# Kernel tuning notes

Hardware: AMD Instinct MI355X
Metric: run time of the kernel (lower is better)

## Reference

```python
import jax, jax.numpy as jnp
import numpy as np

H = 16  # num heads

def setup_inputs() -> dict:
    key = jax.random.key(0)
    k1, k2, k3 = jax.random.split(key, 3)
    B, L, D = 2, 2048, 1024
    x = jax.random.normal(k1, (B, L, D), dtype=jnp.float32)
    # torch Linear weight is [out,in]; we store transposed [in,out] so y = x @ W
    w_qkv = jax.random.normal(k2, (D, 3 * D), dtype=jnp.float32) * (D ** -0.5)
    w_proj = jax.random.normal(k3, (D, D), dtype=jnp.float32) * (D ** -0.5)
    return {"x": x, "w_qkv": w_qkv, "w_proj": w_proj, "num_prefix_tokens": 256}

def _prefix_causal_mask(L: int, M: int):
    # True = masked. Strict upper triangle (causal), then text rows (M:) may
    # see ALL prefix columns (:M).
    mask = jnp.triu(jnp.ones((L, L), dtype=bool), k=1)
    mask = mask.at[M:, :M].set(False)
    return mask

def reference(x, w_qkv, w_proj, num_prefix_tokens):
    B, L, D = x.shape
    d = D // H
    scale = d ** -0.5
    qkv = (x @ w_qkv).reshape(B, L, 3, H, d)
    q = jnp.transpose(qkv[:, :, 0], (0, 2, 1, 3))  # [B,H,L,d]
    k = jnp.transpose(qkv[:, :, 1], (0, 2, 1, 3))
    v = jnp.transpose(qkv[:, :, 2], (0, 2, 1, 3))
    logits = jnp.einsum("bhqd,bhkd->bhqk", q, k) * scale  # [B,H,L,L]
    mask = _prefix_causal_mask(L, num_prefix_tokens)
    logits = jnp.where(mask[None, None], -jnp.inf, logits)
    attn = jax.nn.softmax(logits, axis=-1)
    out = jnp.einsum("bhqk,bhkd->bhqd", attn, v)  # [B,H,L,d]
    out = jnp.transpose(out, (0, 2, 1, 3)).reshape(B, L, D)
    return out @ w_proj
```

## Files before the change

kernel.cpp:

```cpp
#include <hip/hip_runtime.h>
#include <hip/hip_bf16.h>

#define BATCH   2
#define L_SEQ   2048
#define DMODEL  1024
#define NHEADS  16
#define DHEAD   64
#define SEG     (BATCH*NHEADS*L_SEQ*DHEAD)

typedef __attribute__((ext_vector_type(8)))  short bf16x8;
typedef __attribute__((ext_vector_type(4)))  float f32x4;
typedef __attribute__((ext_vector_type(16))) float f32x16;

__device__ __forceinline__ unsigned short f2b(float f) {
    unsigned int u = __float_as_uint(f);
    return (unsigned short)((u + 0x7FFFu + ((u >> 16) & 1u)) >> 16);
}
__device__ __forceinline__ unsigned int pk2(float a, float b) {
    __hip_bfloat162 h = __float22bfloat162_rn(make_float2(a, b));
    return *(unsigned int*)&h;
}
__device__ __forceinline__ void glds16(const unsigned short* g, unsigned short* l) {
    __builtin_amdgcn_global_load_lds(
        (const __attribute__((address_space(1))) unsigned int*)g,
        (__attribute__((address_space(3))) unsigned int*)l, 16, 0, 0);
}

__device__ __forceinline__ void tcast64(const float* __restrict__ in,
                                        unsigned short* __restrict__ out,
                                        int K, int N, int bx, int by, int t) {
    __shared__ unsigned short T[64][65];
    const int k0 = by * 64, n0 = bx * 64;
    const int r = t >> 4, c4 = (t & 15) * 4;
#pragma unroll
    for (int rep = 0; rep < 4; ++rep) {
        int kk = rep * 16 + r;
        float4 f = *(const float4*)&in[(size_t)(k0 + kk) * N + n0 + c4];
        T[kk][c4 + 0] = f2b(f.x);
        T[kk][c4 + 1] = f2b(f.y);
        T[kk][c4 + 2] = f2b(f.z);
        T[kk][c4 + 3] = f2b(f.w);
    }
    __syncthreads();
#pragma unroll
    for (int rep = 0; rep < 4; ++rep) {
        int nn = rep * 16 + r;
        ushort4 o;
        o.x = T[c4 + 0][nn];
        o.y = T[c4 + 1][nn];
        o.z = T[c4 + 2][nn];
        o.w = T[c4 + 3][nn];
        *(ushort4*)&out[(size_t)(n0 + nn) * K + k0 + c4] = o;
    }
}

__global__ __launch_bounds__(256)
void prep(const float* __restrict__ x, const float* __restrict__ wqkv,
          const float* __restrict__ wproj, unsigned short* __restrict__ xb,
          unsigned short* __restrict__ wqkvT, unsigned short* __restrict__ wprojT) {
    const int id = blockIdx.x, t = threadIdx.x;
    if (id < 4096) {
        int i = id * 1024 + t * 4;
        float4 f = *(const float4*)&x[i];
        ushort4 o;
        o.x = f2b(f.x); o.y = f2b(f.y); o.z = f2b(f.z); o.w = f2b(f.w);
        *(ushort4*)&xb[i] = o;
    } else if (id < 4864) {
        int lid = id - 4096;
        tcast64(wqkv, wqkvT, DMODEL, 3 * DMODEL, lid % 48, lid / 48, t);
    } else {
        int lid = id - 4864;
        tcast64(wproj, wprojT, DMODEL, DMODEL, lid & 15, lid >> 4, t);
    }
}

__global__ __launch_bounds__(256)
void gemm_qkv(const unsigned short* __restrict__ A, const unsigned short* __restrict__ Bt,
              unsigned short* __restrict__ Cb) {
    __shared__ unsigned short SLDS[2 * 128 * 128];

    const int t = threadIdx.x;
    const int lane = t & 63, wave = t >> 6;
    const int quad = lane >> 4, l16 = lane & 15;
    const int wm = (wave >> 1) * 64, wn = (wave & 1) * 64;
    const int id = blockIdx.y * gridDim.x + blockIdx.x;
    const int xcd = id & 7, sq = id >> 3;
    const int m0 = (xcd * 4 + sq / 24) * 128;
    const int n0 = (sq % 24) * 128;
    const bool vrole = (n0 >= 2048);

    const int gsw = (lane & 7) ^ (lane >> 3);
    const unsigned short* ga[4];
    const unsigned short* gb[4];
    int ldA[4], ldB[4];
#pragma unroll
    for (int i = 0; i < 4; ++i) {
        int row = wave * 32 + i * 8 + (lane >> 3);
        ga[i] = &A[(size_t)(m0 + row) * DMODEL + gsw * 8];
        gb[i] = &Bt[(size_t)(n0 + row) * DMODEL + gsw * 8];
        ldA[i] = (wave * 32 + i * 8) * 64;
        ldB[i] = 8192 + (wave * 32 + i * 8) * 64;
    }
    const int sx = l16 & 7;

    f32x4 acc[4][4];
#pragma unroll
    for (int i = 0; i < 4; ++i)
#pragma unroll
        for (int j = 0; j < 4; ++j)
#pragma unroll
            for (int r = 0; r < 4; ++r) acc[i][j][r] = 0.0f;

#pragma unroll
    for (int i = 0; i < 4; ++i) {
        glds16(ga[i], &SLDS[ldA[i]]);
        glds16(gb[i], &SLDS[ldB[i]]);
    }
    __syncthreads();

    int cur = 0;
    for (int kt = 0; kt < 16; ++kt) {
        if (kt < 15) {
            const int ko = (kt + 1) * 64;
            unsigned short* dst = &SLDS[(cur ^ 1) * 16384];
#pragma unroll
            for (int i = 0; i < 4; ++i) {
                glds16(ga[i] + ko, dst + ldA[i]);
                glds16(gb[i] + ko, dst + ldB[i]);
            }
        }
        const unsigned short* Asm = &SLDS[cur * 16384];
        const unsigned short* Bsm = Asm + 8192;
#pragma unroll
        for (int s = 0; s < 2; ++s) {
            bf16x8 af[4], bfr[4];
#pragma unroll
            for (int i = 0; i < 4; ++i)
                af[i] = *(const bf16x8*)&Asm[(wm + i * 16 + l16) * 64 + ((4 * s + quad) ^ sx) * 8];
#pragma unroll
            for (int j = 0; j < 4; ++j)
                bfr[j] = *(const bf16x8*)&Bsm[(wn + j * 16 + l16) * 64 + ((4 * s + quad) ^ sx) * 8];
            __builtin_amdgcn_s_setprio(1);
            if (!vrole) {
#pragma unroll
                for (int i = 0; i < 4; ++i)
#pragma unroll
                    for (int j = 0; j < 4; ++j)
                        acc[i][j] = __builtin_amdgcn_mfma_f32_16x16x32_bf16(af[i], bfr[j], acc[i][j], 0, 0, 0);
            } else {
#pragma unroll
                for (int i = 0; i < 4; ++i)
#pragma unroll
                    for (int j = 0; j < 4; ++j)
                        acc[i][j] = __builtin_amdgcn_mfma_f32_16x16x32_bf16(bfr[j], af[i], acc[i][j], 0, 0, 0);
            }
            __builtin_amdgcn_s_setprio(0);
        }
        __syncthreads();
        cur ^= 1;
    }

    const float qscale = 0.1803368801111244f;
    const float scl = (!vrole && n0 < 1024) ? qscale : 1.0f;
#pragma unroll
    for (int i = 0; i < 4; ++i)
#pragma unroll
        for (int r = 0; r < 4; ++r) {
#pragma unroll
            for (int j = 0; j < 4; ++j) {
                int row_l, col_l;
                if (!vrole) {
                    row_l = wm + i * 16 + quad * 4 + r;
                    col_l = wn + j * 16 + l16;
                } else {
                    row_l = wn + j * 16 + quad * 4 + r;
                    col_l = wm + i * 16 + l16;
                }
                int key = row_l & 7;
                SLDS[row_l * 128 + (((col_l >> 3) ^ key) * 8) + (col_l & 7)] =
                    f2b(acc[i][j][r] * scl);
            }
        }
    __syncthreads();

    const int s0 = n0 >> 10;
    const int bb = m0 >> 11;
#pragma unroll
    for (int it = 0; it < 4; ++it) {
        int row = it * 32 + (t >> 3);
        int c = t & 7;
        int key = row & 7;
        bf16x8 v0 = *(const bf16x8*)&SLDS[row * 128 + ((c ^ key) * 8)];
        bf16x8 v1 = *(const bf16x8*)&SLDS[row * 128 + (((c + 8) ^ key) * 8)];
        if (!vrole) {
            int token = m0 + row, lp = token & (L_SEQ - 1);
            int n_a = n0 + c * 8,        h_a = (n_a >> 6) & 15, d_a = n_a & 63;
            int n_b = n0 + (c + 8) * 8,  h_b = (n_b >> 6) & 15, d_b = n_b & 63;
            size_t base = (size_t)s0 * SEG;
            *(bf16x8*)&Cb[base + (((size_t)(bb * NHEADS + h_a) * L_SEQ + lp) * DHEAD) + d_a] = v0;
            *(bf16x8*)&Cb[base + (((size_t)(bb * NHEADS + h_b) * L_SEQ + lp) * DHEAD) + d_b] = v1;
        } else {
            int fr = (n0 - 2048) + row;
            int h = fr >> 6, dd = fr & 63;
            int lp0 = (m0 & (L_SEQ - 1));
            size_t base = 2 * (size_t)SEG +
                          (((size_t)(bb * NHEADS + h) * DHEAD + dd) * L_SEQ) + lp0;
            *(bf16x8*)&Cb[base + c * 8]       = v0;
            *(bf16x8*)&Cb[base + (c + 8) * 8] = v1;
        }
    }
}

__global__ __launch_bounds__(256)
void gemm_proj(const unsigned short* __restrict__ A, const unsigned short* __restrict__ Bt,
               float* __restrict__ Cf) {
    __shared__ unsigned short SLDS[2 * 128 * 128];

    const int t = threadIdx.x;
    const int lane = t & 63, wave = t >> 6;
    const int quad = lane >> 4, l16 = lane & 15;
    const int wm = (wave >> 1) * 64, wn = (wave & 1) * 64;
    const int id = blockIdx.y * gridDim.x + blockIdx.x;
    const int xcd = id & 7, sq = id >> 3;
    const int m0 = (xcd * 4 + (sq >> 3)) * 128;
    const int n0 = (sq & 7) * 128;

    const int gsw = (lane & 7) ^ (lane >> 3);
    const unsigned short* ga[4];
    const unsigned short* gb[4];
    int ldA[4], ldB[4];
#pragma unroll
    for (int i = 0; i < 4; ++i) {
        int row = wave * 32 + i * 8 + (lane >> 3);
        ga[i] = &A[(size_t)(m0 + row) * DMODEL + gsw * 8];
        gb[i] = &Bt[(size_t)(n0 + row) * DMODEL + gsw * 8];
        ldA[i] = (wave * 32 + i * 8) * 64;
        ldB[i] = 8192 + (wave * 32 + i * 8) * 64;
    }
    const int sx = l16 & 7;

    f32x4 acc[4][4];
#pragma unroll
    for (int i = 0; i < 4; ++i)
#pragma unroll
        for (int j = 0; j < 4; ++j)
#pragma unroll
            for (int r = 0; r < 4; ++r) acc[i][j][r] = 0.0f;

#pragma unroll
    for (int i = 0; i < 4; ++i) {
        glds16(ga[i], &SLDS[ldA[i]]);
        glds16(gb[i], &SLDS[ldB[i]]);
    }
    __syncthreads();

    int cur = 0;
    for (int kt = 0; kt < 16; ++kt) {
        if (kt < 15) {
            const int ko = (kt + 1) * 64;
            unsigned short* dst = &SLDS[(cur ^ 1) * 16384];
#pragma unroll
            for (int i = 0; i < 4; ++i) {
                glds16(ga[i] + ko, dst + ldA[i]);
                glds16(gb[i] + ko, dst + ldB[i]);
            }
        }
        const unsigned short* Asm = &SLDS[cur * 16384];
        const unsigned short* Bsm = Asm + 8192;
#pragma unroll
        for (int s = 0; s < 2; ++s) {
            bf16x8 af[4], bfr[4];
#pragma unroll
            for (int i = 0; i < 4; ++i)
                af[i] = *(const bf16x8*)&Asm[(wm + i * 16 + l16) * 64 + ((4 * s + quad) ^ sx) * 8];
#pragma unroll
            for (int j = 0; j < 4; ++j)
                bfr[j] = *(const bf16x8*)&Bsm[(wn + j * 16 + l16) * 64 + ((4 * s + quad) ^ sx) * 8];
            __builtin_amdgcn_s_setprio(1);
#pragma unroll
            for (int i = 0; i < 4; ++i)
#pragma unroll
                for (int j = 0; j < 4; ++j)
                    acc[i][j] = __builtin_amdgcn_mfma_f32_16x16x32_bf16(af[i], bfr[j], acc[i][j], 0, 0, 0);
            __builtin_amdgcn_s_setprio(0);
        }
        __syncthreads();
        cur ^= 1;
    }

#pragma unroll
    for (int i = 0; i < 4; ++i)
#pragma unroll
        for (int r = 0; r < 4; ++r) {
            int row = m0 + wm + i * 16 + quad * 4 + r;
#pragma unroll
            for (int j = 0; j < 4; ++j)
                Cf[(size_t)row * DMODEL + n0 + wn + j * 16 + l16] = acc[i][j][r];
        }
}

__global__ __launch_bounds__(512)
void attn_mfma(const unsigned short* __restrict__ Qg, const unsigned short* __restrict__ Kg,
               const unsigned short* __restrict__ Vg, unsigned short* __restrict__ Ao) {
    __shared__ unsigned short SLDS[32768];
    __shared__ float Rex[128];
    unsigned short* Ksm = SLDS;
    unsigned short* Vsm = SLDS + 8192;
    unsigned short* Psm = SLDS + 16384;

    const int t = threadIdx.x;
    const int lane = t & 63, wave = t >> 6;
    const int l31 = lane & 31, hi = lane >> 5;
    const int bh = blockIdx.x & 31;
    const int Qt = 15 - (blockIdx.x >> 5);
    const int q0 = Qt * 128;
    const int qh = wave & 3, kp = wave >> 2;
    const int wq0 = q0 + qh * 32;
    const int nstrip = Qt + 1;
    const int b = bh >> 4, h = bh & 15;
    const size_t qkbase = (size_t)bh * L_SEQ * DHEAD;
    const size_t vbase  = (size_t)bh * DHEAD * L_SEQ;

    bf16x8 bq[4];
#pragma unroll
    for (int ks = 0; ks < 4; ++ks)
        bq[ks] = *(const bf16x8*)&Qg[qkbase + (size_t)(wq0 + l31) * DHEAD + ks * 16 + hi * 8];

    const int kc0 = t & 7,  kr0 = (t >> 3) * 2;
    const int vc0 = t & 15, vd0 = (t >> 4) * 2;

    unsigned short* Pw = Psm + wave * 2048;

    f32x16 O0, O1;
#pragma unroll
    for (int r = 0; r < 16; ++r) { O0[r] = 0.0f; O1[r] = 0.0f; }
    float rs = 0.0f;

    bf16x8 gk[2], gv[2];
#pragma unroll
    for (int i = 0; i < 2; ++i) {
        gk[i] = *(const bf16x8*)&Kg[qkbase + (size_t)(kr0 + i) * DHEAD + kc0 * 8];
        gv[i] = *(const bf16x8*)&Vg[vbase + (size_t)(vd0 + i) * L_SEQ + vc0 * 8];
    }

    for (int s = 0; s < nstrip; ++s) {
        __syncthreads();
#pragma unroll
        for (int i = 0; i < 2; ++i) {
            *(bf16x8*)&Ksm[(kc0 * 128 + ((kr0 + i) ^ kc0)) * 8] = gk[i];
            *(bf16x8*)&Vsm[(vc0 * 64 + ((vd0 + i) ^ vc0)) * 8] = gv[i];
        }
        if (s + 1 < nstrip) {
            const int kn = (s + 1) * 128;
#pragma unroll
            for (int i = 0; i < 2; ++i) {
                gk[i] = *(const bf16x8*)&Kg[qkbase + (size_t)(kn + kr0 + i) * DHEAD + kc0 * 8];
                gv[i] = *(const bf16x8*)&Vg[vbase + (size_t)(vd0 + i) * L_SEQ + kn + vc0 * 8];
            }
        }
        __syncthreads();

        const int keybase = s * 128 + kp * 64;
        if (keybase <= wq0 + 31) {
            f32x16 ST[2];
            __builtin_amdgcn_s_setprio(1);
#pragma unroll
            for (int kh = 0; kh < 2; ++kh) {
#pragma unroll
                for (int r = 0; r < 16; ++r) ST[kh][r] = 0.0f;
#pragma unroll
                for (int ks = 0; ks < 4; ++ks) {
                    const int c = ks * 2 + hi;
                    const int rk = kp * 64 + kh * 32 + l31;
                    bf16x8 a = *(const bf16x8*)&Ksm[(c * 128 + (rk ^ c)) * 8];
                    ST[kh] = __builtin_amdgcn_mfma_f32_32x32x16_bf16(a, bq[ks], ST[kh], 0, 0, 0);
                }
            }
            __builtin_amdgcn_s_setprio(0);

            if (keybase + 63 > wq0) {
                const int qg = wq0 + l31;
#pragma unroll
                for (int kh = 0; kh < 2; ++kh)
#pragma unroll
                    for (int r = 0; r < 16; ++r) {
                        int keyg = keybase + kh * 32 + (r & 3) + 8 * (r >> 2) + 4 * hi;
                        if (keyg > qg) ST[kh][r] = -1e30f;
                    }
            }

#pragma unroll
            for (int kh = 0; kh < 2; ++kh)
#pragma unroll
                for (int g = 0; g < 4; ++g) {
                    float p0 = __builtin_amdgcn_exp2f(ST[kh][4 * g + 0]);
                    float p1 = __builtin_amdgcn_exp2f(ST[kh][4 * g + 1]);
                    float p2 = __builtin_amdgcn_exp2f(ST[kh][4 * g + 2]);
                    float p3 = __builtin_amdgcn_exp2f(ST[kh][4 * g + 3]);
                    rs += (p0 + p1) + (p2 + p3);
                    const int c = kh * 4 + g;
                    *(uint2*)&Pw[(c * 32 + (l31 ^ c)) * 8 + hi * 4] =
                        make_uint2(pk2(p0, p1), pk2(p2, p3));
                }

            __builtin_amdgcn_s_setprio(1);
#pragma unroll
            for (int ks = 0; ks < 4; ++ks) {
                const int cp = ks * 2 + hi;
                const int cv = kp * 8 + cp;
                bf16x8 pa = *(const bf16x8*)&Pw[(cp * 32 + (l31 ^ cp)) * 8];
                bf16x8 v0 = *(const bf16x8*)&Vsm[(cv * 64 + (l31 ^ cv)) * 8];
                bf16x8 v1 = *(const bf16x8*)&Vsm[(cv * 64 + ((32 + l31) ^ cv)) * 8];
                O0 = __builtin_amdgcn_mfma_f32_32x32x16_bf16(pa, v0, O0, 0, 0, 0);
                O1 = __builtin_amdgcn_mfma_f32_32x32x16_bf16(pa, v1, O1, 0, 0, 0);
            }
            __builtin_amdgcn_s_setprio(0);
        }
    }

    rs += __shfl_xor(rs, 32, 64);

    __syncthreads();
    float* Oex = (float*)SLDS;
    if (kp == 1) {
#pragma unroll
        for (int r = 0; r < 16; ++r) {
            int qloc = (r & 3) + 8 * (r >> 2) + 4 * hi;
            Oex[qh * 2048 + qloc * 64 + l31]      = O0[r];
            Oex[qh * 2048 + qloc * 64 + 32 + l31] = O1[r];
        }
        if (hi == 0) Rex[qh * 32 + l31] = rs;
    }
    __syncthreads();
    if (kp == 0) {
        float rs_tot = rs + Rex[qh * 32 + l31];
        float linv = 1.0f / rs_tot;
        float lf[16];
#pragma unroll
        for (int r = 0; r < 16; ++r) {
            int qloc = (r & 3) + 8 * (r >> 2) + 4 * hi;
            O0[r] += Oex[qh * 2048 + qloc * 64 + l31];
            O1[r] += Oex[qh * 2048 + qloc * 64 + 32 + l31];
            lf[r] = __shfl(linv, qloc, 32);
        }
#pragma unroll
        for (int r = 0; r < 16; ++r) {
            int qloc = (r & 3) + 8 * (r >> 2) + 4 * hi;
            int token = wq0 + qloc;
            size_t ob = ((size_t)(b * L_SEQ + token)) * DMODEL + h * DHEAD;
            Ao[ob + l31]      = f2b(O0[r] * lf[r]);
            Ao[ob + 32 + l31] = f2b(O1[r] * lf[r]);
        }
    }
}

extern "C" void kernel_launch(void* const* d_in, const int* in_sizes, int n_in,
                              void* d_out, int out_size, void* d_ws, size_t ws_size,
                              hipStream_t stream) {
    const float* x      = (const float*)d_in[0];
    const float* w_qkv  = (const float*)d_in[1];
    const float* w_proj = (const float*)d_in[2];
    float* out = (float*)d_out;

    unsigned short* ws     = (unsigned short*)d_ws;
    unsigned short* xb     = ws;
    unsigned short* wqkvT  = xb + 4194304;
    unsigned short* wprojT = wqkvT + 3145728;
    unsigned short* qkv    = wprojT + 1048576;
    unsigned short* ao     = qkv + 3 * (size_t)SEG;

    prep<<<5120, 256, 0, stream>>>(x, w_qkv, w_proj, xb, wqkvT, wprojT);

    gemm_qkv<<<dim3(24, 32), 256, 0, stream>>>(xb, wqkvT, qkv);

    attn_mfma<<<512, 512, 0, stream>>>(qkv, qkv + SEG, qkv + 2 * (size_t)SEG, ao);

    gemm_proj<<<dim3(8, 32), 256, 0, stream>>>(ao, wprojT, out);
}
```

Measured before the change: 163.1 us.

## Use four-stage K-chunk pipeline with vmcnt waits in QKV and proj GEMMs

Both GEMM kernels move from a double-buffered 64-wide K tile to a four-slot ring of 32-wide K tiles. Loads run three stages ahead and completion is tracked with explicit s_waitcnt vmcnt counters plus raw barriers instead of __syncthreads. This is meant to hide global-to-LDS latency and cut the full barrier drain on every iteration. In exchange it adds a correctness risk from hand-tuned wait counts and an extra redundant load at the tail, and the LDS swizzle and addressing are changed to match the new 32-wide rows.

```diff
diff --git a/kernel.cpp b/kernel.cpp
--- a/kernel.cpp
+++ b/kernel.cpp
@@ -25,6 +25,8 @@
         (const __attribute__((address_space(1))) unsigned int*)g,
         (__attribute__((address_space(3))) unsigned int*)l, 16, 0, 0);
 }
+
+#define VMCNT(n) asm volatile("s_waitcnt vmcnt(" #n ")" ::: "memory")
 
 __device__ __forceinline__ void tcast64(const float* __restrict__ in,
                                         unsigned short* __restrict__ out,
@@ -77,7 +79,7 @@
 __global__ __launch_bounds__(256)
 void gemm_qkv(const unsigned short* __restrict__ A, const unsigned short* __restrict__ Bt,
               unsigned short* __restrict__ Cb) {
-    __shared__ unsigned short SLDS[2 * 128 * 128];
+    __shared__ unsigned short SLDS[32768];
 
     const int t = threadIdx.x;
     const int lane = t & 63, wave = t >> 6;
@@ -89,19 +91,19 @@
     const int n0 = (sq % 24) * 128;
     const bool vrole = (n0 >= 2048);
 
-    const int gsw = (lane & 7) ^ (lane >> 3);
-    const unsigned short* ga[4];
-    const unsigned short* gb[4];
-    int ldA[4], ldB[4];
-#pragma unroll
-    for (int i = 0; i < 4; ++i) {
-        int row = wave * 32 + i * 8 + (lane >> 3);
-        ga[i] = &A[(size_t)(m0 + row) * DMODEL + gsw * 8];
-        gb[i] = &Bt[(size_t)(n0 + row) * DMODEL + gsw * 8];
-        ldA[i] = (wave * 32 + i * 8) * 64;
-        ldB[i] = 8192 + (wave * 32 + i * 8) * 64;
-    }
-    const int sx = l16 & 7;
+    const int gch = (lane & 3) ^ ((lane >> 2) & 3) ^ ((lane >> 4) & 3);
+    const unsigned short* gA[2];
+    const unsigned short* gB[2];
+    int ldA[2], ldB[2];
+#pragma unroll
+    for (int j = 0; j < 2; ++j) {
+        int row = j * 64 + (t >> 2);
+        gA[j] = &A [(size_t)(m0 + row) * DMODEL + gch * 8];
+        gB[j] = &Bt[(size_t)(n0 + row) * DMODEL + gch * 8];
+        ldA[j] = j * 2048 + wave * 512;
+        ldB[j] = 4096 + j * 2048 + wave * 512;
+    }
+    const int skey = (l16 ^ (l16 >> 2)) & 3;
 
     f32x4 acc[4][4];
 #pragma unroll
@@ -112,54 +114,57 @@
             for (int r = 0; r < 4; ++r) acc[i][j][r] = 0.0f;
 
 #pragma unroll
-    for (int i = 0; i < 4; ++i) {
-        glds16(ga[i], &SLDS[ldA[i]]);
-        glds16(gb[i], &SLDS[ldB[i]]);
-    }
+    for (int s = 0; s < 3; ++s) {
+        const int sb = s * 8192, ko = s * 32;
+#pragma unroll
+        for (int j = 0; j < 2; ++j) {
+            glds16(gA[j] + ko, &SLDS[sb + ldA[j]]);
+            glds16(gB[j] + ko, &SLDS[sb + ldB[j]]);
+        }
+    }
+    VMCNT(8);
+    __builtin_amdgcn_s_barrier();
+
+#pragma unroll 4
+    for (int kt = 0; kt < 32; ++kt) {
+        const int sb = (kt & 3) * 8192;
+        bf16x8 af[4], bfr[4];
+#pragma unroll
+        for (int i = 0; i < 4; ++i)
+            af[i] = *(const bf16x8*)&SLDS[sb + (wm + i * 16 + l16) * 32 + ((quad ^ skey) * 8)];
+#pragma unroll
+        for (int j = 0; j < 4; ++j)
+            bfr[j] = *(const bf16x8*)&SLDS[sb + 4096 + (wn + j * 16 + l16) * 32 + ((quad ^ skey) * 8)];
+        {
+            const int wb = ((kt + 3) & 3) * 8192;
+            const int ko = (kt < 29 ? kt + 3 : 31) * 32;
+#pragma unroll
+            for (int j = 0; j < 2; ++j) {
+                glds16(gA[j] + ko, &SLDS[wb + ldA[j]]);
+                glds16(gB[j] + ko, &SLDS[wb + ldB[j]]);
+            }
+        }
+        VMCNT(8);
+        __builtin_amdgcn_s_setprio(1);
+        if (!vrole) {
+#pragma unroll
+            for (int i = 0; i < 4; ++i)
+#pragma unroll
+                for (int j = 0; j < 4; ++j)
+                    acc[i][j] = __builtin_amdgcn_mfma_f32_16x16x32_bf16(af[i], bfr[j], acc[i][j], 0, 0, 0);
+        } else {
+#pragma unroll
+            for (int i = 0; i < 4; ++i)
+#pragma unroll
+                for (int j = 0; j < 4; ++j)
+                    acc[i][j] = __builtin_amdgcn_mfma_f32_16x16x32_bf16(bfr[j], af[i], acc[i][j], 0, 0, 0);
+        }
+        __builtin_amdgcn_s_setprio(0);
+        __builtin_amdgcn_s_barrier();
+    }
+
+    VMCNT(0);
     __syncthreads();
-
-    int cur = 0;
-    for (int kt = 0; kt < 16; ++kt) {
-        if (kt < 15) {
-            const int ko = (kt + 1) * 64;
-            unsigned short* dst = &SLDS[(cur ^ 1) * 16384];
-#pragma unroll
-            for (int i = 0; i < 4; ++i) {
-                glds16(ga[i] + ko, dst + ldA[i]);
-                glds16(gb[i] + ko, dst + ldB[i]);
-            }
-        }
-        const unsigned short* Asm = &SLDS[cur * 16384];
-        const unsigned short* Bsm = Asm + 8192;
-#pragma unroll
-        for (int s = 0; s < 2; ++s) {
-            bf16x8 af[4], bfr[4];
-#pragma unroll
-            for (int i = 0; i < 4; ++i)
-                af[i] = *(const bf16x8*)&Asm[(wm + i * 16 + l16) * 64 + ((4 * s + quad) ^ sx) * 8];
-#pragma unroll
-            for (int j = 0; j < 4; ++j)
-                bfr[j] = *(const bf16x8*)&Bsm[(wn + j * 16 + l16) * 64 + ((4 * s + quad) ^ sx) * 8];
-            __builtin_amdgcn_s_setprio(1);
-            if (!vrole) {
-#pragma unroll
-                for (int i = 0; i < 4; ++i)
-#pragma unroll
-                    for (int j = 0; j < 4; ++j)
-                        acc[i][j] = __builtin_amdgcn_mfma_f32_16x16x32_bf16(af[i], bfr[j], acc[i][j], 0, 0, 0);
-            } else {
-#pragma unroll
-                for (int i = 0; i < 4; ++i)
-#pragma unroll
-                    for (int j = 0; j < 4; ++j)
-                        acc[i][j] = __builtin_amdgcn_mfma_f32_16x16x32_bf16(bfr[j], af[i], acc[i][j], 0, 0, 0);
-            }
-            __builtin_amdgcn_s_setprio(0);
-        }
-        __syncthreads();
-        cur ^= 1;
-    }
-
     const float qscale = 0.1803368801111244f;
     const float scl = (!vrole && n0 < 1024) ? qscale : 1.0f;
 #pragma unroll
@@ -214,7 +219,7 @@
 __global__ __launch_bounds__(256)
 void gemm_proj(const unsigned short* __restrict__ A, const unsigned short* __restrict__ Bt,
                float* __restrict__ Cf) {
-    __shared__ unsigned short SLDS[2 * 128 * 128];
+    __shared__ unsigned short SLDS[32768];
 
     const int t = threadIdx.x;
     const int lane = t & 63, wave = t >> 6;
@@ -225,19 +230,19 @@
     const int m0 = (xcd * 4 + (sq >> 3)) * 128;
     const int n0 = (sq & 7) * 128;
 
-    const int gsw = (lane & 7) ^ (lane >> 3);
-    const unsigned short* ga[4];
-    const unsigned short* gb[4];
-    int ldA[4], ldB[4];
-#pragma unroll
-    for (int i = 0; i < 4; ++i) {
-        int row = wave * 32 + i * 8 + (lane >> 3);
-        ga[i] = &A[(size_t)(m0 + row) * DMODEL + gsw * 8];
-        gb[i] = &Bt[(size_t)(n0 + row) * DMODEL + gsw * 8];
-        ldA[i] = (wave * 32 + i * 8) * 64;
-        ldB[i] = 8192 + (wave * 32 + i * 8) * 64;
-    }
-    const int sx = l16 & 7;
+    const int gch = (lane & 3) ^ ((lane >> 2) & 3) ^ ((lane >> 4) & 3);
+    const unsigned short* gA[2];
+    const unsigned short* gB[2];
+    int ldA[2], ldB[2];
+#pragma unroll
+    for (int j = 0; j < 2; ++j) {
+        int row = j * 64 + (t >> 2);
+        gA[j] = &A [(size_t)(m0 + row) * DMODEL + gch * 8];
+        gB[j] = &Bt[(size_t)(n0 + row) * DMODEL + gch * 8];
+        ldA[j] = j * 2048 + wave * 512;
+        ldB[j] = 4096 + j * 2048 + wave * 512;
+    }
+    const int skey = (l16 ^ (l16 >> 2)) & 3;
 
     f32x4 acc[4][4];
 #pragma unroll
@@ -248,46 +253,48 @@
             for (int r = 0; r < 4; ++r) acc[i][j][r] = 0.0f;
 
 #pragma unroll
-    for (int i = 0; i < 4; ++i) {
-        glds16(ga[i], &SLDS[ldA[i]]);
-        glds16(gb[i], &SLDS[ldB[i]]);
-    }
-    __syncthreads();
-
-    int cur = 0;
-    for (int kt = 0; kt < 16; ++kt) {
-        if (kt < 15) {
-            const int ko = (kt + 1) * 64;
-            unsigned short* dst = &SLDS[(cur ^ 1) * 16384];
-#pragma unroll
-            for (int i = 0; i < 4; ++i) {
-                glds16(ga[i] + ko, dst + ldA[i]);
-                glds16(gb[i] + ko, dst + ldB[i]);
-            }
-        }
-        const unsigned short* Asm = &SLDS[cur * 16384];
-        const unsigned short* Bsm = Asm + 8192;
-#pragma unroll
-        for (int s = 0; s < 2; ++s) {
-            bf16x8 af[4], bfr[4];
-#pragma unroll
-            for (int i = 0; i < 4; ++i)
-                af[i] = *(const bf16x8*)&Asm[(wm + i * 16 + l16) * 64 + ((4 * s + quad) ^ sx) * 8];
+    for (int s = 0; s < 3; ++s) {
+        const int sb = s * 8192, ko = s * 32;
+#pragma unroll
+        for (int j = 0; j < 2; ++j) {
+            glds16(gA[j] + ko, &SLDS[sb + ldA[j]]);
+            glds16(gB[j] + ko, &SLDS[sb + ldB[j]]);
+        }
+    }
+    VMCNT(8);
+    __builtin_amdgcn_s_barrier();
+
+#pragma unroll 4
+    for (int kt = 0; kt < 32; ++kt) {
+        const int sb = (kt & 3) * 8192;
+        bf16x8 af[4], bfr[4];
+#pragma unroll
+        for (int i = 0; i < 4; ++i)
+            af[i] = *(const bf16x8*)&SLDS[sb + (wm + i * 16 + l16) * 32 + ((quad ^ skey) * 8)];
+#pragma unroll
+        for (int j = 0; j < 4; ++j)
+            bfr[j] = *(const bf16x8*)&SLDS[sb + 4096 + (wn + j * 16 + l16) * 32 + ((quad ^ skey) * 8)];
+        {
+            const int wb = ((kt + 3) & 3) * 8192;
+            const int ko = (kt < 29 ? kt + 3 : 31) * 32;
+#pragma unroll
+            for (int j = 0; j < 2; ++j) {
+                glds16(gA[j] + ko, &SLDS[wb + ldA[j]]);
+                glds16(gB[j] + ko, &SLDS[wb + ldB[j]]);
+            }
+        }
+        VMCNT(8);
+        __builtin_amdgcn_s_setprio(1);
+#pragma unroll
+        for (int i = 0; i < 4; ++i)
 #pragma unroll
             for (int j = 0; j < 4; ++j)
-                bfr[j] = *(const bf16x8*)&Bsm[(wn + j * 16 + l16) * 64 + ((4 * s + quad) ^ sx) * 8];
-            __builtin_amdgcn_s_setprio(1);
-#pragma unroll
-            for (int i = 0; i < 4; ++i)
-#pragma unroll
-                for (int j = 0; j < 4; ++j)
-                    acc[i][j] = __builtin_amdgcn_mfma_f32_16x16x32_bf16(af[i], bfr[j], acc[i][j], 0, 0, 0);
-            __builtin_amdgcn_s_setprio(0);
-        }
-        __syncthreads();
-        cur ^= 1;
-    }
-
+                acc[i][j] = __builtin_amdgcn_mfma_f32_16x16x32_bf16(af[i], bfr[j], acc[i][j], 0, 0, 0);
+        __builtin_amdgcn_s_setprio(0);
+        __builtin_amdgcn_s_barrier();
+    }
+
+    VMCNT(0);
 #pragma unroll
     for (int i = 0; i < 4; ++i)
 #pragma unroll
```

Result: slower. 167.0 us (+2.4%).
